# Kernel optimization log

Measured on AMD Instinct MI355X. Metric: run time of the kernel, lower is better.

The kernel has to match this reference:

```python
import jax, jax.numpy as jnp
import numpy as np

B, N, F, U, FE, T, E = 2, 50000, 256, 256, 128, 3, 131072


def setup_inputs() -> dict:
    key = jax.random.key(0)
    ks = jax.random.split(key, 7)
    features = jax.random.normal(ks[0], (B, N, F), dtype=jnp.float32)
    edge_idx = jax.random.randint(ks[1], (T, E), 0, B * N, dtype=jnp.int32)  # flattened (b*N+n)
    edge_feats = jax.random.normal(ks[2], (T, E, FE), dtype=jnp.float32)
    W_gate = jax.random.normal(ks[3], (F, U), dtype=jnp.float32) * (1.0 / np.sqrt(F))
    W_gate_e = jax.random.normal(ks[4], (T, FE, U), dtype=jnp.float32) * (1.0 / np.sqrt(FE))
    W_dense = jax.random.normal(ks[5], (T, FE, U), dtype=jnp.float32) * (1.0 / np.sqrt(FE))
    b_dense = jax.random.normal(ks[6], (T, U), dtype=jnp.float32) * 0.01
    return {"features": features, "edge_idx": edge_idx, "edge_feats": edge_feats,
            "W_gate": W_gate, "W_gate_e": W_gate_e, "W_dense": W_dense, "b_dense": b_dense}


def reference(features, edge_idx, edge_feats, W_gate, W_gate_e, W_dense, b_dense):
    b, n, f = features.shape
    u = W_gate.shape[1]
    # shared gate Dense (no bias) applied to all node features; flattened over (B,N)
    src_gated = features.reshape(b * n, f) @ W_gate                      # [B*N, U]
    # per-edge-type gate/value transforms, vectorized over edge types
    gate_e = jnp.einsum('tef,tfu->teu', edge_feats, W_gate_e)            # [T, E, U]
    val_e = jnp.einsum('tef,tfu->teu', edge_feats, W_dense) + b_dense[:, None, :]
    gate = jax.nn.sigmoid(src_gated[edge_idx] + gate_e)                  # gather node gate per edge
    msgs = val_e * gate                                                  # [T, E, U]
    out = jnp.zeros((b * n, u), features.dtype)
    out = out.at[edge_idx.reshape(-1)].add(msgs.reshape(-1, u))          # scatter-add over all edge types
    return out.reshape(b, n, u)
```

## Files before the change

kernel.cpp:

```cpp
#include <hip/hip_runtime.h>
#include <math.h>

#define M1 100000
#define FF 256
#define UU 256
#define FED 128
#define TT 3
#define EE 131072
#define EPB 32
#define TPT 8
#define TPT1 5
#define EPA 32
#define SCAN_B 98

typedef __attribute__((ext_vector_type(8))) short short8;
typedef __attribute__((ext_vector_type(4))) short short4v;
typedef __attribute__((ext_vector_type(4))) float f32x4;

static __device__ __forceinline__ ushort f2bf(float x) {
    union { __bf16 b; ushort u; } c; c.b = (__bf16)x; return c.u;
}
static __device__ __forceinline__ float bf2f(ushort h) {
    union { uint u; float f; } c; c.u = ((uint)h) << 16;
    return c.f;
}

__global__ __launch_bounds__(256) void k_prep(const float* __restrict__ Wg,
                                              const float* __restrict__ Wge,
                                              const float* __restrict__ Wde,
                                              short* __restrict__ WtG,
                                              short* __restrict__ WtGe,
                                              short* __restrict__ WtDe) {
    const int idx = blockIdx.x * 256 + threadIdx.x;
    if (idx < 65536) {
        const int n = idx >> 8, k = idx & 255;
        WtG[n * 256 + k] = (short)f2bf(Wg[k * 256 + n]);
    } else {
        int j = idx - 65536;
        const float* src = Wge;
        short* dst = WtGe;
        if (j >= 98304) { j -= 98304; src = Wde; dst = WtDe; }
        const int t = j >> 15, rem = j & 32767;
        const int n = rem >> 7, k = rem & 127;
        dst[t * 32768 + n * 128 + k] = (short)f2bf(src[t * 32768 + k * 256 + n]);
    }
}

__global__ __launch_bounds__(1024, 4) void k1_srcgate(const float* __restrict__ feats,
                                                      const short* __restrict__ WtG,
                                                      ushort* __restrict__ sg) {
    __shared__ char As[2][32 * 512];
    const int tid = threadIdx.x, lane = tid & 63, wid = tid >> 6;
    const int tile0 = blockIdx.x * TPT1;

    const int col = wid * 16 + (lane & 15);
    const int ksl = (lane >> 4) * 8;
    short8 wb[8];
#pragma unroll
    for (int ks = 0; ks < 8; ++ks)
        wb[ks] = *(const short8*)(WtG + col * 256 + ks * 32 + ksl);

    const int erow = tid >> 5, ekc = tid & 31;
    float4 pf0, pf1;
    {
        const float* src = feats + ((size_t)(tile0 * 32) + erow) * FF + ekc * 8;
        pf0 = *(const float4*)(src);
        pf1 = *(const float4*)(src + 4);
    }

    for (int it = 0; it < TPT1; ++it) {
        const int p = it & 1;
        {
            short8 v;
            v[0]=(short)f2bf(pf0.x); v[1]=(short)f2bf(pf0.y); v[2]=(short)f2bf(pf0.z); v[3]=(short)f2bf(pf0.w);
            v[4]=(short)f2bf(pf1.x); v[5]=(short)f2bf(pf1.y); v[6]=(short)f2bf(pf1.z); v[7]=(short)f2bf(pf1.w);
            int byte = erow * 512 + ekc * 16;
            byte ^= (erow & 7) << 4;
            *(short8*)(As[p] + byte) = v;
        }
        __syncthreads();

        if (it + 1 < TPT1) {
            const float* src = feats + ((size_t)((tile0 + it + 1) * 32) + erow) * FF + ekc * 8;
            pf0 = *(const float4*)(src);
            pf1 = *(const float4*)(src + 4);
        }

        f32x4 acc[2];
#pragma unroll
        for (int m = 0; m < 2; ++m) acc[m] = (f32x4){0.f, 0.f, 0.f, 0.f};
#pragma unroll
        for (int ks = 0; ks < 8; ++ks) {
#pragma unroll
            for (int m = 0; m < 2; ++m) {
                const int row = m * 16 + (lane & 15);
                int byte = row * 512 + ks * 64 + (lane >> 4) * 16;
                byte ^= (row & 7) << 4;
                const short8 a = *(const short8*)(As[p] + byte);
                acc[m] = __builtin_amdgcn_mfma_f32_16x16x32_bf16(a, wb[ks], acc[m], 0, 0, 0);
            }
        }

        const int r0 = (tile0 + it) * 32;
#pragma unroll
        for (int m = 0; m < 2; ++m) {
#pragma unroll
            for (int r = 0; r < 4; ++r) {
                const int row = m * 16 + (lane >> 4) * 4 + r;
                sg[(size_t)(r0 + row) * UU + col] = f2bf(acc[m][r]);
            }
        }
    }
}

__global__ __launch_bounds__(256) void k_hist(const int* __restrict__ eidx,
                                              int* __restrict__ cnt) {
    const int idx = blockIdx.x * 256 + threadIdx.x;
    atomicAdd(&cnt[(idx >> 17) * M1 + eidx[idx]], 1);
}

__global__ __launch_bounds__(1024) void k_scan1(int* __restrict__ cnt,
                                                int* __restrict__ part) {
    const int t = blockIdx.x / SCAN_B, b = blockIdx.x % SCAN_B;
    const int i = b * 1024 + threadIdx.x;
    __shared__ int s[1024];
    const int v = (i < M1) ? cnt[t * M1 + i] : 0;
    s[threadIdx.x] = v;
    __syncthreads();
    for (int off = 1; off < 1024; off <<= 1) {
        const int x = (threadIdx.x >= off) ? s[threadIdx.x - off] : 0;
        __syncthreads();
        s[threadIdx.x] += x;
        __syncthreads();
    }
    if (i < M1) cnt[t * M1 + i] = s[threadIdx.x] - v;
    if (threadIdx.x == 1023) part[blockIdx.x] = s[1023];
}

__global__ __launch_bounds__(128) void k_scan2(int* __restrict__ part) {
    const int t = blockIdx.x;
    __shared__ int s[128];
    const int v = (threadIdx.x < SCAN_B) ? part[t * SCAN_B + threadIdx.x] : 0;
    s[threadIdx.x] = v;
    __syncthreads();
    for (int off = 1; off < 128; off <<= 1) {
        const int x = (threadIdx.x >= off) ? s[threadIdx.x - off] : 0;
        __syncthreads();
        s[threadIdx.x] += x;
        __syncthreads();
    }
    if (threadIdx.x < SCAN_B) part[t * SCAN_B + threadIdx.x] = s[threadIdx.x] - v;
}

__global__ __launch_bounds__(1024) void k_scan3(int* __restrict__ cnt,
                                                const int* __restrict__ part) {
    const int t = blockIdx.x / SCAN_B, b = blockIdx.x % SCAN_B;
    const int i = b * 1024 + threadIdx.x;
    if (i < M1) cnt[t * M1 + i] += part[blockIdx.x];
}

__global__ __launch_bounds__(256) void k_scatter(const int* __restrict__ eidx,
                                                 int* __restrict__ cur,
                                                 int* __restrict__ sorted,
                                                 int* __restrict__ snode) {
    const int idx = blockIdx.x * 256 + threadIdx.x;
    const int t = idx >> 17;
    const int v = eidx[idx];
    const int slot = atomicAdd(&cur[t * M1 + v], 1);
    sorted[t * EE + slot] = idx & (EE - 1);
    snode[t * EE + slot]  = v;
}

__global__ __launch_bounds__(1024, 4) void k2_msgs(const float* __restrict__ efeat,
                                                   const short* __restrict__ WtGe,
                                                   const short* __restrict__ WtDe,
                                                   const float* __restrict__ bd,
                                                   const ushort* __restrict__ sg,
                                                   const int* __restrict__ sorted,
                                                   const int* __restrict__ snode,
                                                   ushort* __restrict__ msgs) {
    __shared__ char As[2][EPB * 256];
    const int tid = threadIdx.x, lane = tid & 63, wid = tid >> 6;
    const int t = blockIdx.y;
    const int tile0 = blockIdx.x * TPT;

    const int col = wid * 16 + (lane & 15);
    const int ksl = (lane >> 4) * 8;
    const short* Bg = WtGe + t * 32768;
    const short* Bd = WtDe + t * 32768;
    short8 wg[4], wv[4];
#pragma unroll
    for (int ks = 0; ks < 4; ++ks) {
        wg[ks] = *(const short8*)(Bg + col * 128 + ks * 32 + ksl);
        wv[ks] = *(const short8*)(Bd + col * 128 + ks * 32 + ksl);
    }
    const float bias = bd[t * UU + col];

    const int erow = tid >> 5, ekc = tid & 31;
    const int rbase = (lane >> 4) * 4;

    float4 pf_e;
    {
        const int base = t * EE + tile0 * EPB;
        const int se = sorted[base + erow];
        pf_e = *(const float4*)(efeat + ((size_t)t * EE + se) * FED + ekc * 4);
    }

    for (int it = 0; it < TPT; ++it) {
        const int p = it & 1;
        const int e0 = (tile0 + it) * EPB;
        const int base = t * EE + e0;

        {
            short4v v;
            v[0] = (short)f2bf(pf_e.x); v[1] = (short)f2bf(pf_e.y);
            v[2] = (short)f2bf(pf_e.z); v[3] = (short)f2bf(pf_e.w);
            int byte = erow * 256 + ekc * 8;
            byte ^= (erow & 7) << 4;
            *(short4v*)(As[p] + byte) = v;
        }
        __syncthreads();

        ushort sgv[8];
#pragma unroll
        for (int j = 0; j < 8; ++j) {
            const int row = (j >> 2) * 16 + rbase + (j & 3);
            const int nd = snode[base + row];
            sgv[j] = sg[(size_t)nd * UU + col];
        }
        if (it + 1 < TPT) {
            const int nbase = t * EE + (tile0 + it + 1) * EPB;
            const int se = sorted[nbase + erow];
            pf_e = *(const float4*)(efeat + ((size_t)t * EE + se) * FED + ekc * 4);
        }

        f32x4 accg[2], accv[2];
#pragma unroll
        for (int m = 0; m < 2; ++m) {
            accg[m] = (f32x4){0.f, 0.f, 0.f, 0.f};
            accv[m] = (f32x4){bias, bias, bias, bias};
        }
#pragma unroll
        for (int ks = 0; ks < 4; ++ks) {
#pragma unroll
            for (int m = 0; m < 2; ++m) {
                const int row = m * 16 + (lane & 15);
                int byte = row * 256 + ks * 64 + (lane >> 4) * 16;
                byte ^= (row & 7) << 4;
                const short8 a = *(const short8*)(As[p] + byte);
                accg[m] = __builtin_amdgcn_mfma_f32_16x16x32_bf16(a, wg[ks], accg[m], 0, 0, 0);
                accv[m] = __builtin_amdgcn_mfma_f32_16x16x32_bf16(a, wv[ks], accv[m], 0, 0, 0);
            }
        }

#pragma unroll
        for (int m = 0; m < 2; ++m) {
#pragma unroll
            for (int r = 0; r < 4; ++r) {
                const float sgf = bf2f(sgv[m * 4 + r]);
                const float e = __expf(-(sgf + accg[m][r]));
                const float g = __builtin_amdgcn_rcpf(1.f + e);
                const float msg = accv[m][r] * g;
                const int row = m * 16 + rbase + r;
                msgs[((size_t)t * EE + e0 + row) * UU + col] = f2bf(msg);
            }
        }
    }
}

__global__ __launch_bounds__(256, 8) void k3_reduce(const int* __restrict__ cnt,
                                                    const ushort* __restrict__ msgs,
                                                    float* __restrict__ out) {
    const int tid = threadIdx.x, lane = tid & 63, w = tid >> 6;
    const int v = blockIdx.x * 4 + w;
    float a0 = 0.f, a1 = 0.f, a2 = 0.f, a3 = 0.f;
#pragma unroll
    for (int t = 0; t < TT; ++t) {
        const int end   = cnt[t * M1 + v];
        const int start = (v == 0) ? 0 : cnt[t * M1 + v - 1];
        const ushort* base = msgs + (size_t)t * EE * UU + lane * 4;
        int e = start;
        for (; e + 1 < end; e += 2) {
            const uint2 d0 = *(const uint2*)(base + (size_t)e * UU);
            const uint2 d1 = *(const uint2*)(base + (size_t)(e + 1) * UU);
            a0 += bf2f((ushort)(d0.x & 0xffff)) + bf2f((ushort)(d1.x & 0xffff));
            a1 += bf2f((ushort)(d0.x >> 16))    + bf2f((ushort)(d1.x >> 16));
            a2 += bf2f((ushort)(d0.y & 0xffff)) + bf2f((ushort)(d1.y & 0xffff));
            a3 += bf2f((ushort)(d0.y >> 16))    + bf2f((ushort)(d1.y >> 16));
        }
        if (e < end) {
            const uint2 d0 = *(const uint2*)(base + (size_t)e * UU);
            a0 += bf2f((ushort)(d0.x & 0xffff));
            a1 += bf2f((ushort)(d0.x >> 16));
            a2 += bf2f((ushort)(d0.y & 0xffff));
            a3 += bf2f((ushort)(d0.y >> 16));
        }
    }
    float4 o; o.x = a0; o.y = a1; o.z = a2; o.w = a3;
    *(float4*)(out + (size_t)v * UU + lane * 4) = o;
}

__global__ __launch_bounds__(256, 4) void k2_edges(const int* __restrict__ eidx,
                                                   const float* __restrict__ efeat,
                                                   const short* __restrict__ WtGe,
                                                   const short* __restrict__ WtDe,
                                                   const float* __restrict__ bd,
                                                   const ushort* __restrict__ sg,
                                                   const int* __restrict__ sorted,
                                                   float* __restrict__ out) {
    __shared__ char As[EPA * 256];
    __shared__ ushort sgl[EPA][260];
    __shared__ int nds[EPA];
    const int tid = threadIdx.x, lane = tid & 63, wid = tid >> 6;
    const int t = blockIdx.y;
    const int e0 = blockIdx.x * EPA;
    const int* sortedT = sorted + t * EE + e0;
    const int* eidxT   = eidx + t * EE;

    if (tid < EPA) nds[tid] = eidxT[sortedT[tid]];
#pragma unroll
    for (int j = 0; j < 2; ++j) {
        const int chunk = j * 256 + tid;
        const int row = chunk >> 4, kc = chunk & 15;
        const int se = sortedT[row];
        const float* src = efeat + ((size_t)t * EE + se) * FED + kc * 8;
        const float4 f0 = *(const float4*)(src);
        const float4 f1 = *(const float4*)(src + 4);
        short8 v;
        v[0]=(short)f2bf(f0.x); v[1]=(short)f2bf(f0.y); v[2]=(short)f2bf(f0.z); v[3]=(short)f2bf(f0.w);
        v[4]=(short)f2bf(f1.x); v[5]=(short)f2bf(f1.y); v[6]=(short)f2bf(f1.z); v[7]=(short)f2bf(f1.w);
        int byte = row * 256 + kc * 16;
        byte ^= (row & 7) << 4;
        *(short8*)(As + byte) = v;
    }
    __syncthreads();
#pragma unroll
    for (int j = 0; j < 16; ++j) {
        const int item = j * 256 + tid;
        const int row = item >> 7, c2 = item & 127;
        const uint v = *(const uint*)(sg + (size_t)nds[row] * UU + c2 * 2);
        *(uint*)&sgl[row][c2 * 2] = v;
    }
    const short* Bg = WtGe + t * 32768;
    const short* Bd = WtDe + t * 32768;
    const int nb = wid * 64;
    f32x4 accg[2][4], accv[2][4];
#pragma unroll
    for (int m = 0; m < 2; ++m)
#pragma unroll
        for (int n = 0; n < 4; ++n) {
            accg[m][n] = (f32x4){0.f, 0.f, 0.f, 0.f};
            accv[m][n] = (f32x4){0.f, 0.f, 0.f, 0.f};
        }
#pragma unroll
    for (int ks = 0; ks < 4; ++ks) {
        short8 a[2];
#pragma unroll
        for (int m = 0; m < 2; ++m) {
            const int row = m * 16 + (lane & 15);
            int byte = row * 256 + ks * 64 + (lane >> 4) * 16;
            byte ^= (row & 7) << 4;
            a[m] = *(const short8*)(As + byte);
        }
#pragma unroll
        for (int n = 0; n < 4; ++n) {
            const int col = nb + n * 16 + (lane & 15);
            const int koff = ks * 32 + (lane >> 4) * 8;
            const short8 bg = *(const short8*)(Bg + col * 128 + koff);
            const short8 bv = *(const short8*)(Bd + col * 128 + koff);
#pragma unroll
            for (int m = 0; m < 2; ++m) {
                accg[m][n] = __builtin_amdgcn_mfma_f32_16x16x32_bf16(a[m], bg, accg[m][n], 0, 0, 0);
                accv[m][n] = __builtin_amdgcn_mfma_f32_16x16x32_bf16(a[m], bv, accv[m][n], 0, 0, 0);
            }
        }
    }
    __syncthreads();
    float bias[4];
#pragma unroll
    for (int n = 0; n < 4; ++n) bias[n] = bd[t * UU + nb + n * 16 + (lane & 15)];
#pragma unroll
    for (int m = 0; m < 2; ++m) {
        const int ebase = m * 16 + (lane >> 4) * 4;
        int node[4];
#pragma unroll
        for (int r = 0; r < 4; ++r) node[r] = nds[ebase + r];
#pragma unroll
        for (int n = 0; n < 4; ++n) {
            const int col = nb + n * 16 + (lane & 15);
            float carry = 0.f;
#pragma unroll
            for (int r = 0; r < 4; ++r) {
                const float sgv = bf2f(sgl[ebase + r][col]);
                const float e = __expf(-(sgv + accg[m][n][r]));
                const float g = __builtin_amdgcn_rcpf(1.f + e);
                carry += (accv[m][n][r] + bias[n]) * g;
                if (r == 3 || node[r + 1] != node[r]) {
                    atomicAdd(&out[(size_t)node[r] * UU + col], carry);
                    carry = 0.f;
                }
            }
        }
    }
}

extern "C" void kernel_launch(void* const* d_in, const int* in_sizes, int n_in,
                              void* d_out, int out_size, void* d_ws, size_t ws_size,
                              hipStream_t stream) {
    const float* feats = (const float*)d_in[0];
    const int*   eidx  = (const int*)d_in[1];
    const float* efeat = (const float*)d_in[2];
    const float* Wg    = (const float*)d_in[3];
    const float* Wge   = (const float*)d_in[4];
    const float* Wde   = (const float*)d_in[5];
    const float* bd    = (const float*)d_in[6];
    float* out = (float*)d_out;

    char* ws = (char*)d_ws;
    size_t off = 0;
    auto alloc = [&](size_t bytes) { char* p = ws + off; off = (off + bytes + 511) & ~(size_t)511; return p; };
    ushort* sg   = (ushort*)alloc((size_t)M1 * UU * 2);
    short* WtG   = (short*)alloc(256 * 256 * 2);
    short* WtGe  = (short*)alloc((size_t)TT * FED * UU * 2);
    short* WtDe  = (short*)alloc((size_t)TT * FED * UU * 2);
    int* cnt     = (int*)alloc((size_t)TT * M1 * 4);
    int* part    = (int*)alloc(4096);
    int* sorted  = (int*)alloc((size_t)TT * EE * 4);
    int* snode   = (int*)alloc((size_t)TT * EE * 4);
    const size_t small_needed = off;
    ushort* msgs = (ushort*)alloc((size_t)TT * EE * UU * 2);
    const size_t big_needed = off;

    hipMemsetAsync(cnt, 0, (size_t)TT * M1 * 4, stream);
    k_prep<<<262144 / 256, 256, 0, stream>>>(Wg, Wge, Wde, WtG, WtGe, WtDe);
    k1_srcgate<<<M1 / 32 / TPT1, 1024, 0, stream>>>(feats, WtG, sg);

    k_hist<<<(TT * EE) / 256, 256, 0, stream>>>(eidx, cnt);
    k_scan1<<<TT * SCAN_B, 1024, 0, stream>>>(cnt, part);
    k_scan2<<<TT, 128, 0, stream>>>(part);
    k_scan3<<<TT * SCAN_B, 1024, 0, stream>>>(cnt, part);
    k_scatter<<<(TT * EE) / 256, 256, 0, stream>>>(eidx, cnt, sorted, snode);

    if (ws_size >= big_needed) {
        k2_msgs<<<dim3((EE / EPB) / TPT, TT), 1024, 0, stream>>>(efeat, WtGe, WtDe, bd,
                                                                 (const ushort*)sg, sorted, snode, msgs);
        k3_reduce<<<M1 / 4, 256, 0, stream>>>(cnt, (const ushort*)msgs, out);
    } else if (ws_size >= small_needed) {
        hipMemsetAsync(d_out, 0, (size_t)out_size * sizeof(float), stream);
        k2_edges<<<dim3(EE / EPA, TT), 256, 0, stream>>>(eidx, efeat, WtGe, WtDe, bd,
                                                         (const ushort*)sg, sorted, out);
    }
}
```

Baseline: 347.1 us.

## Make srcgate one tile per block and shrink msgs tiles-per-block

k1_srcgate goes from five 32-row tiles per block with a double-buffered prefetch pipeline to one tile per block, launching 3125 blocks instead of 625. Each block now loads its weights once, converts one tile and does one MFMA pass. k2_msgs drops from 8 tiles per block to 2, giving four times as many blocks, and its loop is unrolled. The aim is more parallelism and occupancy across the GPU. The cost is reloading the weight fragments per block and losing the load/compute overlap.

```diff
diff --git a/kernel.cpp b/kernel.cpp
--- a/kernel.cpp
+++ b/kernel.cpp
@@ -8,8 +8,7 @@
 #define TT 3
 #define EE 131072
 #define EPB 32
-#define TPT 8
-#define TPT1 5
+#define TPT 2
 #define EPA 32
 #define SCAN_B 98
 
@@ -49,66 +48,54 @@
 __global__ __launch_bounds__(1024, 4) void k1_srcgate(const float* __restrict__ feats,
                                                       const short* __restrict__ WtG,
                                                       ushort* __restrict__ sg) {
-    __shared__ char As[2][32 * 512];
+    __shared__ char As[32 * 512];
     const int tid = threadIdx.x, lane = tid & 63, wid = tid >> 6;
-    const int tile0 = blockIdx.x * TPT1;
+    const int r0 = blockIdx.x * 32;
 
     const int col = wid * 16 + (lane & 15);
     const int ksl = (lane >> 4) * 8;
+
+    const int erow = tid >> 5, ekc = tid & 31;
+    const float* src = feats + ((size_t)r0 + erow) * FF + ekc * 8;
+    const float4 pf0 = *(const float4*)(src);
+    const float4 pf1 = *(const float4*)(src + 4);
+
     short8 wb[8];
 #pragma unroll
     for (int ks = 0; ks < 8; ++ks)
         wb[ks] = *(const short8*)(WtG + col * 256 + ks * 32 + ksl);
 
-    const int erow = tid >> 5, ekc = tid & 31;
-    float4 pf0, pf1;
     {
-        const float* src = feats + ((size_t)(tile0 * 32) + erow) * FF + ekc * 8;
-        pf0 = *(const float4*)(src);
-        pf1 = *(const float4*)(src + 4);
-    }
-
-    for (int it = 0; it < TPT1; ++it) {
-        const int p = it & 1;
-        {
-            short8 v;
-            v[0]=(short)f2bf(pf0.x); v[1]=(short)f2bf(pf0.y); v[2]=(short)f2bf(pf0.z); v[3]=(short)f2bf(pf0.w);
-            v[4]=(short)f2bf(pf1.x); v[5]=(short)f2bf(pf1.y); v[6]=(short)f2bf(pf1.z); v[7]=(short)f2bf(pf1.w);
-            int byte = erow * 512 + ekc * 16;
-            byte ^= (erow & 7) << 4;
-            *(short8*)(As[p] + byte) = v;
-        }
-        __syncthreads();
-
-        if (it + 1 < TPT1) {
-            const float* src = feats + ((size_t)((tile0 + it + 1) * 32) + erow) * FF + ekc * 8;
-            pf0 = *(const float4*)(src);
-            pf1 = *(const float4*)(src + 4);
-        }
-
-        f32x4 acc[2];
-#pragma unroll
-        for (int m = 0; m < 2; ++m) acc[m] = (f32x4){0.f, 0.f, 0.f, 0.f};
-#pragma unroll
-        for (int ks = 0; ks < 8; ++ks) {
-#pragma unroll
-            for (int m = 0; m < 2; ++m) {
-                const int row = m * 16 + (lane & 15);
-                int byte = row * 512 + ks * 64 + (lane >> 4) * 16;
-                byte ^= (row & 7) << 4;
-                const short8 a = *(const short8*)(As[p] + byte);
-                acc[m] = __builtin_amdgcn_mfma_f32_16x16x32_bf16(a, wb[ks], acc[m], 0, 0, 0);
-            }
-        }
-
-        const int r0 = (tile0 + it) * 32;
+        short8 v;
+        v[0]=(short)f2bf(pf0.x); v[1]=(short)f2bf(pf0.y); v[2]=(short)f2bf(pf0.z); v[3]=(short)f2bf(pf0.w);
+        v[4]=(short)f2bf(pf1.x); v[5]=(short)f2bf(pf1.y); v[6]=(short)f2bf(pf1.z); v[7]=(short)f2bf(pf1.w);
+        int byte = erow * 512 + ekc * 16;
+        byte ^= (erow & 7) << 4;
+        *(short8*)(As + byte) = v;
+    }
+    __syncthreads();
+
+    f32x4 acc[2];
+#pragma unroll
+    for (int m = 0; m < 2; ++m) acc[m] = (f32x4){0.f, 0.f, 0.f, 0.f};
+#pragma unroll
+    for (int ks = 0; ks < 8; ++ks) {
 #pragma unroll
         for (int m = 0; m < 2; ++m) {
-#pragma unroll
-            for (int r = 0; r < 4; ++r) {
-                const int row = m * 16 + (lane >> 4) * 4 + r;
-                sg[(size_t)(r0 + row) * UU + col] = f2bf(acc[m][r]);
-            }
+            const int row = m * 16 + (lane & 15);
+            int byte = row * 512 + ks * 64 + (lane >> 4) * 16;
+            byte ^= (row & 7) << 4;
+            const short8 a = *(const short8*)(As + byte);
+            acc[m] = __builtin_amdgcn_mfma_f32_16x16x32_bf16(a, wb[ks], acc[m], 0, 0, 0);
+        }
+    }
+
+#pragma unroll
+    for (int m = 0; m < 2; ++m) {
+#pragma unroll
+        for (int r = 0; r < 4; ++r) {
+            const int row = m * 16 + (lane >> 4) * 4 + r;
+            sg[(size_t)(r0 + row) * UU + col] = f2bf(acc[m][r]);
         }
     }
 }
@@ -206,6 +193,7 @@
         pf_e = *(const float4*)(efeat + ((size_t)t * EE + se) * FED + ekc * 4);
     }
 
+#pragma unroll
     for (int it = 0; it < TPT; ++it) {
         const int p = it & 1;
         const int e0 = (tile0 + it) * EPB;
@@ -433,7 +421,7 @@
 
     hipMemsetAsync(cnt, 0, (size_t)TT * M1 * 4, stream);
     k_prep<<<262144 / 256, 256, 0, stream>>>(Wg, Wge, Wde, WtG, WtGe, WtDe);
-    k1_srcgate<<<M1 / 32 / TPT1, 1024, 0, stream>>>(feats, WtG, sg);
+    k1_srcgate<<<M1 / 32, 1024, 0, stream>>>(feats, WtG, sg);
 
     k_hist<<<(TT * EE) / 256, 256, 0, stream>>>(eidx, cnt);
     k_scan1<<<TT * SCAN_B, 1024, 0, stream>>>(cnt, part);
```

Result: slower. 398.8 us (+14.9%).
